# Performance work log

Hardware: AMD Instinct MI355X
Metric: run time of the kernel (lower is better)

The kernel has to match this reference:

```python
import jax, jax.numpy as jnp
import numpy as np

N, D = 8192, 768
EPS = 1e-5  # torch LayerNorm default


def setup_inputs() -> dict:
    key = jax.random.key(0)
    ks = jax.random.split(key, 5)
    q = jax.random.normal(ks[0], (N, D), dtype=jnp.float32)
    k = jax.random.normal(ks[1], (N, D), dtype=jnp.float32)
    v = jax.random.normal(ks[2], (N, D), dtype=jnp.float32)
    ln_w = jnp.ones((D,), dtype=jnp.float32)
    ln_b = jnp.zeros((D,), dtype=jnp.float32)
    W_qkv = jax.random.normal(ks[3], (D, D), dtype=jnp.float32) * 0.02
    W_proj = jax.random.normal(ks[4], (D, D), dtype=jnp.float32) * 0.02
    b_proj = jnp.zeros((D,), dtype=jnp.float32)
    return {"q": q, "k": k, "v": v, "ln_w": ln_w, "ln_b": ln_b,
            "W_qkv": W_qkv, "W_proj": W_proj, "b_proj": b_proj}


def reference(q, k, v, ln_w, ln_b, W_qkv, W_proj, b_proj):
    dim = q.shape[-1]
    scale = dim ** (-0.5)

    def ln(x):
        mu = jnp.mean(x, axis=-1, keepdims=True)
        var = jnp.mean((x - mu) ** 2, axis=-1, keepdims=True)
        return (x - mu) * jax.lax.rsqrt(var + EPS) * ln_w + ln_b

    # shared LayerNorm + shared Linear (toto0, no bias) applied to q, k, v
    qn = ln(q) @ W_qkv.T  # [N, D]
    kn = ln(k) @ W_qkv.T
    vn = ln(v) @ W_qkv.T

    attn = jnp.einsum('qc,kc->qk', qn, kn) * scale  # [N, N]
    attn = jax.nn.softmax(attn, axis=-1)
    out = jnp.einsum('qk,kc->qc', attn, vn)  # [N, D]
    out = out @ W_proj.T + b_proj  # proj0
    return out
```

## Files before the change

### kernel.cpp

```cpp
#include <hip/hip_runtime.h>
#include <hip/hip_bf16.h>
#include <stdint.h>

typedef short bf16x8 __attribute__((ext_vector_type(8)));
typedef float f32x4 __attribute__((ext_vector_type(4)));
typedef unsigned short u16;
typedef u16 u16x8 __attribute__((ext_vector_type(8)));

__device__ __forceinline__ u16 f2bf(float x) {
  __hip_bfloat16 h = __float2bfloat16(x);
  return *reinterpret_cast<u16*>(&h);
}
__device__ __forceinline__ float bf2f(u16 v) {
  unsigned u = (unsigned)v << 16;
  return *reinterpret_cast<float*>(&u);
}

__device__ __forceinline__ void gload_lds16(const void* g, const void* lds_base) {
  __builtin_amdgcn_global_load_lds(
      (const __attribute__((address_space(1))) unsigned int*)(uintptr_t)g,
      (__attribute__((address_space(3))) unsigned int*)(uintptr_t)lds_base,
      16, 0, 0);
}

#define BAR() __builtin_amdgcn_s_barrier()

__global__ __launch_bounds__(256) void ln_cast_kernel(
    const float* __restrict__ q, const float* __restrict__ k, const float* __restrict__ v,
    const float* __restrict__ lw, const float* __restrict__ lb, u16* __restrict__ out) {
  int row = blockIdx.x;
  const float* x;
  if (row < 8192) x = q + (size_t)row * 768;
  else if (row < 16384) x = k + (size_t)(row - 8192) * 768;
  else x = v + (size_t)(row - 16384) * 768;
  int t = threadIdx.x;
  __shared__ float red[4];
  __shared__ float red2[4];
  float4 a = (t < 192) ? ((const float4*)x)[t] : make_float4(0.f, 0.f, 0.f, 0.f);
  float s = a.x + a.y + a.z + a.w;
  for (int o = 32; o; o >>= 1) s += __shfl_down(s, o, 64);
  if ((t & 63) == 0) red[t >> 6] = s;
  __syncthreads();
  float mean = (red[0] + red[1] + red[2]) * (1.0f / 768.0f);
  float4 d = make_float4(a.x - mean, a.y - mean, a.z - mean, a.w - mean);
  float vs = (t < 192) ? (d.x * d.x + d.y * d.y + d.z * d.z + d.w * d.w) : 0.f;
  for (int o = 32; o; o >>= 1) vs += __shfl_down(vs, o, 64);
  if ((t & 63) == 0) red2[t >> 6] = vs;
  __syncthreads();
  float var = (red2[0] + red2[1] + red2[2]) * (1.0f / 768.0f);
  float rstd = rsqrtf(var + 1e-5f);
  if (t < 192) {
    float4 wv = ((const float4*)lw)[t];
    float4 bv = ((const float4*)lb)[t];
    ushort4 o;
    o.x = f2bf(d.x * rstd * wv.x + bv.x);
    o.y = f2bf(d.y * rstd * wv.y + bv.y);
    o.z = f2bf(d.z * rstd * wv.z + bv.z);
    o.w = f2bf(d.w * rstd * wv.w + bv.w);
    ((ushort4*)(out + (size_t)row * 768))[t] = o;
  }
}

__global__ __launch_bounds__(256) void cast_f32_bf16(const float* __restrict__ in,
                                                     u16* __restrict__ out, int n4) {
  int i = blockIdx.x * 256 + threadIdx.x;
  if (i < n4) {
    float4 vv = ((const float4*)in)[i];
    ushort4 o;
    o.x = f2bf(vv.x); o.y = f2bf(vv.y); o.z = f2bf(vv.z); o.w = f2bf(vv.w);
    ((ushort4*)out)[i] = o;
  }
}

__global__ __launch_bounds__(256) void zero_f32(float* __restrict__ p, int n) {
  int i = blockIdx.x * 256 + threadIdx.x;
  if (i < n) p[i] = 0.0f;
}

__global__ __launch_bounds__(256) void reduce4_scale(
    const u16* __restrict__ p0, const u16* __restrict__ p1,
    const u16* __restrict__ p2, const u16* __restrict__ p3,
    const float* __restrict__ rowsum, u16* __restrict__ out, int n8) {
  int i = blockIdx.x * 256 + threadIdx.x;
  if (i < n8) {
    float inv = 1.0f / rowsum[i / 96];
    u16x8 a = ((const u16x8*)p0)[i];
    u16x8 b = ((const u16x8*)p1)[i];
    u16x8 c = ((const u16x8*)p2)[i];
    u16x8 d = ((const u16x8*)p3)[i];
    u16x8 o;
#pragma unroll
    for (int j = 0; j < 8; j++)
      o[j] = f2bf((bf2f(a[j]) + bf2f(b[j]) + bf2f(c[j]) + bf2f(d[j])) * inv);
    ((u16x8*)out)[i] = o;
  }
}

__global__ __launch_bounds__(512, 2) void qk_exp_256(
    const u16* __restrict__ A, const u16* __restrict__ B, u16* __restrict__ C,
    float* __restrict__ rowsum, float scale) {
  __shared__ __align__(16) u16 lds[8 * 256 * 32];
  int orig = blockIdx.x;
  int xcd = orig & 7, i = orig >> 3;
  int tm = xcd * 4 + (i & 3), tn = i >> 2;
  const int t = threadIdx.x, l = t & 63, w = t >> 6;
  const int wr = w >> 2, wc = w & 3;
  const int lr = l & 15, lq = l >> 4;
  const int colb = lq * 16;

  f32x4 acc[8][4];
#pragma unroll
  for (int m = 0; m < 8; m++)
#pragma unroll
    for (int n = 0; n < 4; n++) acc[m][n] = (f32x4){0.f, 0.f, 0.f, 0.f};

  const size_t rA0 = (size_t)tm * 256, rB0 = (size_t)tn * 256;

  const char* gsrc[4];
  int ldsoff[4];
#pragma unroll
  for (int idx = 0; idx < 4; idx++) {
    const u16* src = (idx < 2) ? A : B;
    size_t r0 = (idx < 2) ? rA0 : rB0;
    int p = idx & 1;
    int x = p * 8192 + t * 16;
    int r = x >> 6;
    int cb = (x & 63) ^ (((r >> 1) & 3) << 4);
    gsrc[idx] = (const char*)(src + (r0 + r) * 768) + cb;
    ldsoff[idx] = ((idx < 2) ? 0 : 65536) + p * 8192 + w * 1024;
  }
  int offA[2][4], offB[4];
#pragma unroll
  for (int mh = 0; mh < 2; mh++)
#pragma unroll
    for (int mf = 0; mf < 4; mf++) {
      int row = wr * 128 + (mh * 4 + mf) * 16 + lr;
      int x = row * 64 + colb;
      offA[mh][mf] = x ^ (((row >> 1) & 3) << 4);
    }
#pragma unroll
  for (int nf = 0; nf < 4; nf++) {
    int row = wc * 64 + nf * 16 + lr;
    int x = row * 64 + colb;
    offB[nf] = 65536 + (x ^ (((row >> 1) & 3) << 4));
  }

#define SCALL(BUF, TT, IDX)                                                  \
  gload_lds16(gsrc[IDX] + (size_t)(TT) * 64,                                 \
              (const char*)lds + (BUF) * 16384 + ldsoff[IDX])

  auto LOADA = [&](bf16x8 (&aF)[4], int b, int mh) {
#pragma unroll
    for (int mf = 0; mf < 4; mf++)
      aF[mf] = *(const bf16x8*)((const char*)lds + b * 16384 + offA[mh][mf]);
  };
  auto LOADB = [&](bf16x8 (&bF)[4], int b) {
#pragma unroll
    for (int nf = 0; nf < 4; nf++)
      bF[nf] = *(const bf16x8*)((const char*)lds + b * 16384 + offB[nf]);
  };
  auto MM32 = [&](bf16x8 (&aF)[4], bf16x8 (&aG)[4], bf16x8 (&bF)[4]) {
    __builtin_amdgcn_s_setprio(1);
#pragma unroll
    for (int mf = 0; mf < 4; mf++)
#pragma unroll
      for (int nf = 0; nf < 4; nf++)
        acc[mf][nf] = __builtin_amdgcn_mfma_f32_16x16x32_bf16(
            aF[mf], bF[nf], acc[mf][nf], 0, 0, 0);
#pragma unroll
    for (int mf = 0; mf < 4; mf++)
#pragma unroll
      for (int nf = 0; nf < 4; nf++)
        acc[4 + mf][nf] = __builtin_amdgcn_mfma_f32_16x16x32_bf16(
            aG[mf], bF[nf], acc[4 + mf][nf], 0, 0, 0);
    __builtin_amdgcn_s_setprio(0);
  };

#define PHASE(CUR, SBUF, STAGET, DOSTAGE, VMN)                               \
  do {                                                                       \
    bf16x8 aF[4], aG[4], bF[4];                                              \
    LOADA(aF, CUR, 0);                                                       \
    LOADA(aG, CUR, 1);                                                       \
    LOADB(bF, CUR);                                                          \
    if (DOSTAGE) {                                                           \
      SCALL(SBUF, STAGET, 0); SCALL(SBUF, STAGET, 1);                        \
      SCALL(SBUF, STAGET, 2); SCALL(SBUF, STAGET, 3);                        \
    }                                                                        \
    BAR();                                                                   \
    MM32(aF, aG, bF);                                                        \
    if ((VMN) == 8) asm volatile("s_waitcnt vmcnt(8)" ::: "memory");         \
    else if ((VMN) == 4) asm volatile("s_waitcnt vmcnt(4)" ::: "memory");    \
    else if ((VMN) == 0) asm volatile("s_waitcnt vmcnt(0)" ::: "memory");    \
    BAR();                                                                   \
  } while (0)

  SCALL(0, 0, 0); SCALL(0, 0, 1); SCALL(0, 0, 2); SCALL(0, 0, 3);
  SCALL(1, 1, 0); SCALL(1, 1, 1); SCALL(1, 1, 2); SCALL(1, 1, 3);
  SCALL(2, 2, 0); SCALL(2, 2, 1); SCALL(2, 2, 2); SCALL(2, 2, 3);
  asm volatile("s_waitcnt vmcnt(8)" ::: "memory");
  BAR();

  for (int Tb = 0; Tb < 20; Tb += 4) {
    PHASE(0, 3, Tb + 3, 1, 8);
    PHASE(1, 0, Tb + 4, 1, 8);
    PHASE(2, 1, Tb + 5, 1, 8);
    PHASE(3, 2, Tb + 6, 1, 8);
  }
  PHASE(0, 3, 23, 1, 8);
  PHASE(1, 0, 0, 0, 4);
  PHASE(2, 0, 0, 0, 0);
  PHASE(3, 0, 0, 0, -1);

#undef PHASE
#undef SCALL

  float rs[8][4];
#pragma unroll
  for (int m = 0; m < 8; m++)
#pragma unroll
    for (int j = 0; j < 4; j++) rs[m][j] = 0.0f;
  const size_t rowBase = rA0 + (size_t)wr * 128;
  const int colBase = tn * 256 + wc * 64;
#pragma unroll
  for (int mi = 0; mi < 8; mi++) {
    size_t row0 = rowBase + mi * 16 + lq * 4;
#pragma unroll
    for (int nf = 0; nf < 4; nf++) {
      int col = colBase + nf * 16 + lr;
#pragma unroll
      for (int j = 0; j < 4; j++) {
        float e = __expf(acc[mi][nf][j] * scale);
        C[(row0 + j) * 8192 + col] = f2bf(e);
        rs[mi][j] += e;
      }
    }
  }
#pragma unroll
  for (int mi = 0; mi < 8; mi++)
#pragma unroll
    for (int j = 0; j < 4; j++) {
      float r = rs[mi][j];
      r += __shfl_xor(r, 1); r += __shfl_xor(r, 2);
      r += __shfl_xor(r, 4); r += __shfl_xor(r, 8);
      if (lr == 0) atomicAdd(&rowsum[rowBase + mi * 16 + lq * 4 + j], r);
    }
}

template <int MODE>
__global__ __launch_bounds__(256, 2) void gemm_bt(
    const u16* __restrict__ A0, const u16* __restrict__ B0,
    void* __restrict__ Cv0, void* __restrict__ Cv1,
    int M, int N, int K, int lda, int ldb, int ldc,
    float scale, const float* __restrict__ bias, size_t cSplitStride) {
  __shared__ __align__(16) u16 sA[128 * 64];
  __shared__ __align__(16) u16 sB[128 * 64];
  const int z = blockIdx.y;
  const u16* A = A0 + (size_t)z * (size_t)K;
  const u16* B = B0 + (size_t)z * (size_t)K;
  u16* Cb = (z < 2) ? ((u16*)Cv0 + (size_t)z * cSplitStride)
                    : ((u16*)Cv1 + (size_t)(z - 2) * cSplitStride);
  const int nTn = N >> 7;
  int nwg = gridDim.x, orig = blockIdx.x;
  int qq = nwg >> 3, rr = nwg & 7;
  int xcd = orig & 7, loc = orig >> 3;
  int wg = (xcd < rr ? xcd * (qq + 1) : rr * (qq + 1) + (xcd - rr) * qq) + loc;
  int tm = wg / nTn, tn = wg % nTn;

  const int t = threadIdx.x, l = t & 63, w = t >> 6;
  const int wr = w >> 1, wc = w & 1;
  const int lr = l & 15, kg = (l >> 4) << 3;

  f32x4 acc[4][4];
#pragma unroll
  for (int m = 0; m < 4; m++)
#pragma unroll
    for (int n = 0; n < 4; n++) acc[m][n] = (f32x4){0.f, 0.f, 0.f, 0.f};

  const size_t rowA0 = (size_t)tm * 128;
  const size_t rowB0 = (size_t)tn * 128;
  const int nk = K >> 6;
  for (int kt = 0; kt < nk; kt++) {
    const int k0 = kt << 6;
#pragma unroll
    for (int i = 0; i < 4; i++) {
      int chunk = i * 256 + t;
      int row = chunk >> 3;
      int col = (chunk & 7) << 3;
      gload_lds16(A + (rowA0 + row) * lda + k0 + col, (const char*)sA + (i * 256 + w * 64) * 16);
      gload_lds16(B + (rowB0 + row) * ldb + k0 + col, (const char*)sB + (i * 256 + w * 64) * 16);
    }
    __syncthreads();
#pragma unroll
    for (int kk = 0; kk < 2; kk++) {
      bf16x8 af[4], bfv[4];
#pragma unroll
      for (int m = 0; m < 4; m++)
        af[m] = *(const bf16x8*)&sA[(wr * 64 + m * 16 + lr) * 64 + kk * 32 + kg];
#pragma unroll
      for (int n = 0; n < 4; n++)
        bfv[n] = *(const bf16x8*)&sB[(wc * 64 + n * 16 + lr) * 64 + kk * 32 + kg];
#pragma unroll
      for (int m = 0; m < 4; m++)
#pragma unroll
        for (int n = 0; n < 4; n++)
          acc[m][n] = __builtin_amdgcn_mfma_f32_16x16x32_bf16(af[m], bfv[n], acc[m][n], 0, 0, 0);
    }
    __syncthreads();
  }
#pragma unroll
  for (int m = 0; m < 4; m++) {
    int row = tm * 128 + wr * 64 + m * 16 + ((l >> 4) << 2);
#pragma unroll
    for (int n = 0; n < 4; n++) {
      int col = tn * 128 + wc * 64 + n * 16 + lr;
      if (MODE == 2) {
#pragma unroll
        for (int j = 0; j < 4; j++)
          ((float*)Cv0)[(size_t)(row + j) * ldc + col] = acc[m][n][j] + bias[col];
      } else if (MODE == 3 && tm >= 128) {
        ushort4 o;
        o.x = f2bf(acc[m][n][0]); o.y = f2bf(acc[m][n][1]);
        o.z = f2bf(acc[m][n][2]); o.w = f2bf(acc[m][n][3]);
        *(ushort4*)((u16*)Cv1 + (size_t)col * 8192 + (row - 16384)) = o;
      } else {
#pragma unroll
        for (int j = 0; j < 4; j++)
          Cb[(size_t)(row + j) * ldc + col] = f2bf(acc[m][n][j] * scale);
      }
    }
  }
}

extern "C" void kernel_launch(void* const* d_in, const int* in_sizes, int n_in,
                              void* d_out, int out_size, void* d_ws, size_t ws_size,
                              hipStream_t stream) {
  const float* q  = (const float*)d_in[0];
  const float* k  = (const float*)d_in[1];
  const float* v  = (const float*)d_in[2];
  const float* lw = (const float*)d_in[3];
  const float* lb = (const float*)d_in[4];
  const float* Wq = (const float*)d_in[5];
  const float* Wp = (const float*)d_in[6];
  const float* bp = (const float*)d_in[7];

  char* ws = (char*)d_ws;
  size_t off = 0;
  auto alloc = [&](size_t b) { size_t o = off; off += (b + 255) & ~(size_t)255; return o; };
  size_t o_ln = alloc((size_t)24576 * 768 * 2);
  size_t o_pj = alloc((size_t)24576 * 768 * 2);
  size_t o_wq = alloc((size_t)768 * 768 * 2);
  size_t o_wp = alloc((size_t)768 * 768 * 2);
  u16* lnbuf = (u16*)(ws + o_ln);
  u16* pj    = (u16*)(ws + o_pj);
  u16* wqb   = (u16*)(ws + o_wq);
  u16* wpb   = (u16*)(ws + o_wp);
  const size_t NS = (size_t)8192 * 768;
  float* rowsum = (float*)lnbuf;
  u16* p0 = lnbuf + NS;
  u16* p1 = lnbuf + 2 * NS;
  u16* vnT = pj + 2 * NS;
  u16* p2 = (u16*)d_out;
  u16* p3 = p2 + NS;
  size_t fixedEnd = off;
  u16* Sbuf = (u16*)(ws + fixedEnd);

  const float scale = 0.03608439182435161f;

  ln_cast_kernel<<<dim3(24576), dim3(256), 0, stream>>>(q, k, v, lw, lb, lnbuf);
  cast_f32_bf16<<<dim3(576), dim3(256), 0, stream>>>(Wq, wqb, 147456);
  cast_f32_bf16<<<dim3(576), dim3(256), 0, stream>>>(Wp, wpb, 147456);

  gemm_bt<3><<<dim3(1152), dim3(256), 0, stream>>>(lnbuf, wqb, (void*)pj, (void*)vnT,
      24576, 768, 768, 768, 768, 768, 1.0f, (const float*)nullptr, 0);

  zero_f32<<<dim3(32), dim3(256), 0, stream>>>(rowsum, 8192);

  qk_exp_256<<<dim3(1024), dim3(512), 0, stream>>>(pj, pj + NS, Sbuf, rowsum, scale);

  gemm_bt<0><<<dim3(384, 4), dim3(256), 0, stream>>>(
      Sbuf, vnT, (void*)p0, (void*)p2,
      8192, 768, 2048, 8192, 8192, 768, 1.0f, (const float*)nullptr, NS);

  reduce4_scale<<<dim3(3072), dim3(256), 0, stream>>>(p0, p1, p2, p3, rowsum, p0, (int)(NS / 8));

  gemm_bt<2><<<dim3(384), dim3(256), 0, stream>>>(p0, wpb, d_out, d_out,
      8192, 768, 768, 768, 768, 768, 1.0f, bp, 0);
}
```

Baseline: 356.2 us.

## Add dedicated 4-stage pipelined PV GEMM, merge weight casts, drop QK barrier

Replaces the generic gemm_bt for the split-K P·V product with a specialized pv_128 kernel. The new kernel uses a 4-buffer global-to-LDS prefetch ring with swizzled layout, one barrier per K step, and hardcoded sizes. It also fuses the two weight-cast launches into one kernel and removes one barrier per phase in the QK/exp kernel. That last change risks an LDS read/write race if the staging writes overlap buffers still being read.

```diff
diff --git a/kernel.cpp b/kernel.cpp
--- a/kernel.cpp
+++ b/kernel.cpp
@@ -61,15 +61,17 @@
   }
 }
 
-__global__ __launch_bounds__(256) void cast_f32_bf16(const float* __restrict__ in,
-                                                     u16* __restrict__ out, int n4) {
+__global__ __launch_bounds__(256) void cast2_f32_bf16(
+    const float* __restrict__ wa, const float* __restrict__ wb,
+    u16* __restrict__ oa, u16* __restrict__ ob) {
   int i = blockIdx.x * 256 + threadIdx.x;
-  if (i < n4) {
-    float4 vv = ((const float4*)in)[i];
-    ushort4 o;
-    o.x = f2bf(vv.x); o.y = f2bf(vv.y); o.z = f2bf(vv.z); o.w = f2bf(vv.w);
-    ((ushort4*)out)[i] = o;
-  }
+  const float* in = (i < 147456) ? wa : wb;
+  u16* out = (i < 147456) ? oa : ob;
+  int j = (i < 147456) ? i : i - 147456;
+  float4 vv = ((const float4*)in)[j];
+  ushort4 o;
+  o.x = f2bf(vv.x); o.y = f2bf(vv.y); o.z = f2bf(vv.z); o.w = f2bf(vv.w);
+  ((ushort4*)out)[j] = o;
 }
 
 __global__ __launch_bounds__(256) void zero_f32(float* __restrict__ p, int n) {
@@ -186,7 +188,6 @@
       SCALL(SBUF, STAGET, 0); SCALL(SBUF, STAGET, 1);                        \
       SCALL(SBUF, STAGET, 2); SCALL(SBUF, STAGET, 3);                        \
     }                                                                        \
-    BAR();                                                                   \
     MM32(aF, aG, bF);                                                        \
     if ((VMN) == 8) asm volatile("s_waitcnt vmcnt(8)" ::: "memory");         \
     else if ((VMN) == 4) asm volatile("s_waitcnt vmcnt(4)" ::: "memory");    \
@@ -244,6 +245,109 @@
       r += __shfl_xor(r, 4); r += __shfl_xor(r, 8);
       if (lr == 0) atomicAdd(&rowsum[rowBase + mi * 16 + lq * 4 + j], r);
     }
+}
+
+__global__ __launch_bounds__(256, 2) void pv_128(
+    const u16* __restrict__ A, const u16* __restrict__ B,
+    u16* __restrict__ C0, u16* __restrict__ C1) {
+  __shared__ __align__(16) u16 lds[4 * 8192];
+  const int z = blockIdx.y;
+  const int KOFF = z << 11;
+  u16* C = (z < 2) ? C0 + (size_t)z * 6291456 : C1 + (size_t)(z - 2) * 6291456;
+  int orig = blockIdx.x;
+  int wg = (orig & 7) * 48 + (orig >> 3);
+  int tm = wg / 6, tn = wg % 6;
+  const int t = threadIdx.x, l = t & 63, w = t >> 6;
+  const int wr = w >> 1, wc = w & 1;
+  const int lr = l & 15, lq = l >> 4;
+  const int colb = lq * 16;
+
+  f32x4 acc[4][4];
+#pragma unroll
+  for (int m = 0; m < 4; m++)
+#pragma unroll
+    for (int n = 0; n < 4; n++) acc[m][n] = (f32x4){0.f, 0.f, 0.f, 0.f};
+
+  const size_t rA0 = (size_t)tm * 128, rB0 = (size_t)tn * 128;
+
+  const char* gsrc[4];
+  int ldsoff[4];
+#pragma unroll
+  for (int idx = 0; idx < 4; idx++) {
+    const u16* src = (idx < 2) ? A : B;
+    size_t r0 = (idx < 2) ? rA0 : rB0;
+    int p = idx & 1;
+    int x = p * 4096 + t * 16;
+    int r = x >> 6;
+    int cb = (x & 63) ^ (((r >> 1) & 3) << 4);
+    gsrc[idx] = (const char*)(src + (r0 + r) * 8192 + KOFF) + cb;
+    ldsoff[idx] = ((idx < 2) ? 0 : 32768) + p * 4096 + w * 1024;
+  }
+  int offA[4], offB[4];
+#pragma unroll
+  for (int mf = 0; mf < 4; mf++) {
+    int row = wr * 64 + mf * 16 + lr;
+    int x = row * 64 + colb;
+    offA[mf] = x ^ (((row >> 1) & 3) << 4);
+  }
+#pragma unroll
+  for (int nf = 0; nf < 4; nf++) {
+    int row = wc * 64 + nf * 16 + lr;
+    int x = row * 64 + colb;
+    offB[nf] = 32768 + (x ^ (((row >> 1) & 3) << 4));
+  }
+
+#define PSCALL(BUF, TT, IDX)                                                 \
+  gload_lds16(gsrc[IDX] + (size_t)(TT) * 64,                                 \
+              (const char*)lds + (BUF) * 8192 + ldsoff[IDX])
+
+  PSCALL(0, 0, 0); PSCALL(0, 0, 1); PSCALL(0, 0, 2); PSCALL(0, 0, 3);
+  PSCALL(1, 1, 0); PSCALL(1, 1, 1); PSCALL(1, 1, 2); PSCALL(1, 1, 3);
+  PSCALL(2, 2, 0); PSCALL(2, 2, 1); PSCALL(2, 2, 2); PSCALL(2, 2, 3);
+  asm volatile("s_waitcnt vmcnt(8)" ::: "memory");
+  BAR();
+
+#pragma unroll 4
+  for (int T = 0; T < 64; T++) {
+    const int cur = T & 3;
+    bf16x8 aF[4], bF[4];
+#pragma unroll
+    for (int mf = 0; mf < 4; mf++)
+      aF[mf] = *(const bf16x8*)((const char*)lds + cur * 8192 + offA[mf]);
+#pragma unroll
+    for (int nf = 0; nf < 4; nf++)
+      bF[nf] = *(const bf16x8*)((const char*)lds + cur * 8192 + offB[nf]);
+    if (T < 61) {
+      const int nb = (T + 3) & 3;
+      PSCALL(nb, T + 3, 0); PSCALL(nb, T + 3, 1);
+      PSCALL(nb, T + 3, 2); PSCALL(nb, T + 3, 3);
+    }
+    __builtin_amdgcn_s_setprio(1);
+#pragma unroll
+    for (int mf = 0; mf < 4; mf++)
+#pragma unroll
+      for (int nf = 0; nf < 4; nf++)
+        acc[mf][nf] = __builtin_amdgcn_mfma_f32_16x16x32_bf16(
+            aF[mf], bF[nf], acc[mf][nf], 0, 0, 0);
+    __builtin_amdgcn_s_setprio(0);
+    if (T < 61)       asm volatile("s_waitcnt vmcnt(8)" ::: "memory");
+    else if (T == 61) asm volatile("s_waitcnt vmcnt(4)" ::: "memory");
+    else if (T == 62) asm volatile("s_waitcnt vmcnt(0)" ::: "memory");
+    BAR();
+  }
+#undef PSCALL
+
+#pragma unroll
+  for (int mf = 0; mf < 4; mf++) {
+    int row = tm * 128 + wr * 64 + mf * 16 + lq * 4;
+#pragma unroll
+    for (int nf = 0; nf < 4; nf++) {
+      int col = tn * 128 + wc * 64 + nf * 16 + lr;
+#pragma unroll
+      for (int j = 0; j < 4; j++)
+        C[(size_t)(row + j) * 768 + col] = f2bf(acc[mf][nf][j]);
+    }
+  }
 }
 
 template <int MODE>
@@ -367,8 +471,7 @@
   const float scale = 0.03608439182435161f;
 
   ln_cast_kernel<<<dim3(24576), dim3(256), 0, stream>>>(q, k, v, lw, lb, lnbuf);
-  cast_f32_bf16<<<dim3(576), dim3(256), 0, stream>>>(Wq, wqb, 147456);
-  cast_f32_bf16<<<dim3(576), dim3(256), 0, stream>>>(Wp, wpb, 147456);
+  cast2_f32_bf16<<<dim3(1152), dim3(256), 0, stream>>>(Wq, Wp, wqb, wpb);
 
   gemm_bt<3><<<dim3(1152), dim3(256), 0, stream>>>(lnbuf, wqb, (void*)pj, (void*)vnT,
       24576, 768, 768, 768, 768, 768, 1.0f, (const float*)nullptr, 0);
@@ -377,9 +480,7 @@
 
   qk_exp_256<<<dim3(1024), dim3(512), 0, stream>>>(pj, pj + NS, Sbuf, rowsum, scale);
 
-  gemm_bt<0><<<dim3(384, 4), dim3(256), 0, stream>>>(
-      Sbuf, vnT, (void*)p0, (void*)p2,
-      8192, 768, 2048, 8192, 8192, 768, 1.0f, (const float*)nullptr, NS);
+  pv_128<<<dim3(384, 4), dim3(256), 0, stream>>>(Sbuf, vnT, p0, p2);
 
   reduce4_scale<<<dim3(3072), dim3(256), 0, stream>>>(p0, p1, p2, p3, rowsum, p0, (int)(NS / 8));
 
```

Measured after the change: 342.1 us. 1.04x faster.
